# Optimization experiments

Measured on AMD Instinct MI355X. Metric: run time of the kernel, lower is better.

The kernel has to match this reference:

```python
import jax, jax.numpy as jnp
import numpy as np
from jax.scipy.special import logsumexp

B, M, N = 512, 256, 256
ITERS = 20


def setup_inputs() -> dict:
    key = jax.random.key(0)
    k1, = jax.random.split(key, 1)
    scores = jax.random.normal(k1, (B, M, N), dtype=jnp.float32)
    alpha = jnp.ones((1,), dtype=jnp.float32)  # dustbin_weights parameter
    return {"scores": scores, "alpha": alpha, "iters": ITERS}


def reference(scores, alpha, iters):
    b, m, n = scores.shape
    a = alpha.reshape(())
    # Augment with dustbin row/column -> couplings [b, m+1, n+1]
    bins0 = jnp.broadcast_to(a, (b, m, 1))
    bins1 = jnp.broadcast_to(a, (b, 1, n))
    corner = jnp.broadcast_to(a, (b, 1, 1))
    couplings = jnp.concatenate(
        [jnp.concatenate([scores, bins0], axis=2),
         jnp.concatenate([bins1, corner], axis=2)], axis=1)

    ms = jnp.asarray(m, scores.dtype)
    ns = jnp.asarray(n, scores.dtype)
    norm = -jnp.log(ms + ns)  # scalar
    log_mu = jnp.concatenate([jnp.full((m,), norm, scores.dtype),
                              (jnp.log(ns) + norm)[None]])  # [m+1]
    log_nu = jnp.concatenate([jnp.full((n,), norm, scores.dtype),
                              (jnp.log(ms) + norm)[None]])  # [n+1]
    log_mu = jnp.broadcast_to(log_mu[None], (b, m + 1))
    log_nu = jnp.broadcast_to(log_nu[None], (b, n + 1))

    u0 = jnp.zeros_like(log_mu)
    v0 = jnp.zeros_like(log_nu)

    def body(carry, _):
        u, v = carry
        u = log_mu - logsumexp(couplings + v[:, None, :], axis=2)
        v = log_nu - logsumexp(couplings + u[:, :, None], axis=1)
        return (u, v), None

    (u, v), _ = jax.lax.scan(body, (u0, v0), None, length=iters)
    Z = couplings + u[:, :, None] + v[:, None, :]
    return Z - norm
```

## Files before the change

kernel.cpp:

```cpp
#include <hip/hip_runtime.h>


typedef _Float16 half8 __attribute__((ext_vector_type(8)));
typedef float floatx4 __attribute__((ext_vector_type(4)));

constexpr float L2E = 1.4426950408889634f;
constexpr float LN2 = 0.6931471805599453f;

__device__ __forceinline__ float flog2(float x) { return __builtin_amdgcn_logf(x); }
__device__ __forceinline__ float fexp2(float x) { return __builtin_amdgcn_exp2f(x); }

__device__ __forceinline__ float rcp_nr(float d) {
    float r = __builtin_amdgcn_rcpf(d);
    return r * fmaf(-d, r, 2.0f);
}

template <int CTRL>
__device__ __forceinline__ float dpp_add(float x) {
    int y = __builtin_amdgcn_update_dpp(0, __builtin_bit_cast(int, x), CTRL, 0xF, 0xF, true);
    return x + __builtin_bit_cast(float, y);
}
__device__ __forceinline__ float reduce16(float x) {
    x = dpp_add<0xB1>(x);
    x = dpp_add<0x4E>(x);
    x = dpp_add<0x124>(x);
    x = dpp_add<0x128>(x);
    return x;
}
__device__ __forceinline__ float xor16_add(float x) {
    int y = __builtin_amdgcn_ds_swizzle(__builtin_bit_cast(int, x), 0x401F);
    return x + __builtin_bit_cast(float, y);
}

__global__ __launch_bounds__(1024)
__attribute__((amdgpu_waves_per_eu(4, 4)))
void sinkhorn_kernel(const float* __restrict__ scores,
                     const float* __restrict__ alpha_p,
                     const int* __restrict__ iters_p,
                     float* __restrict__ out)
{
    const int bat = blockIdx.x;
    const int t   = threadIdx.x;
    const int a   = t >> 5;
    const int bb  = t & 31;
    const int w   = t >> 6;
    const int l   = t & 63;
    const int g   = (t >> 4) & 3;
    const int l15 = t & 15;

    const float alpha2 = alpha_p[0] * L2E;
    const float A  = fexp2(alpha2);
    const float Cs = fexp2(8.0f - alpha2);
    const int iters = iters_p[0];

    __shared__ __align__(16) unsigned short esT[65536];
    __shared__ __align__(16) unsigned short EUa[272];
    __shared__ __align__(16) unsigned short EVa[272];
    __shared__ __align__(16) float wsU[16];
    __shared__ __align__(16) float wsV[16];

    {
        const float* sp = scores + ((size_t)bat << 16) + ((size_t)a << 11) + (bb << 2);
        half8 cp[8];
        #pragma unroll
        for (int r = 0; r < 8; ++r) {
            const float4 x0 = *reinterpret_cast<const float4*>(sp + (r << 8));
            const float4 x1 = *reinterpret_cast<const float4*>(sp + (r << 8) + 128);
            cp[0][r] = (_Float16)fexp2(x0.x * L2E);
            cp[1][r] = (_Float16)fexp2(x0.y * L2E);
            cp[2][r] = (_Float16)fexp2(x0.z * L2E);
            cp[3][r] = (_Float16)fexp2(x0.w * L2E);
            cp[4][r] = (_Float16)fexp2(x1.x * L2E);
            cp[5][r] = (_Float16)fexp2(x1.y * L2E);
            cp[6][r] = (_Float16)fexp2(x1.z * L2E);
            cp[7][r] = (_Float16)fexp2(x1.w * L2E);
        }
        #pragma unroll
        for (int ci = 0; ci < 8; ++ci) {
            const int col = (ci < 4) ? ((bb << 2) + ci) : (128 + (bb << 2) + ci - 4);
            const int idx = (col << 8) + (((a << 3)) ^ ((col & 7) << 3));
            *reinterpret_cast<half8*>(&esT[idx]) = cp[ci];
        }
    }
    if (t < 256) EVa[t] = 0x3C00;
    if (t < 16)  wsV[t] = 16.0f;
    __syncthreads();

    half8 esA[8];
    {
        const int m16 = (w << 4) + l15;
        #pragma unroll
        for (int s = 0; s < 8; ++s) {
            #pragma unroll
            for (int j = 0; j < 8; ++j) {
                const int col = (s << 5) + (g << 3) + j;
                const unsigned short v =
                    esT[(col << 8) + (m16 ^ ((col & 7) << 3))];
                esA[s][j] = __builtin_bit_cast(_Float16, v);
            }
            asm volatile("" : "+v"(esA[s]));
        }
    }
    half8 esB[8];
    {
        const int cbase = ((w << 4) + l15) << 8;
        const int swq = (l15 & 7) << 3;
        #pragma unroll
        for (int s = 0; s < 8; ++s) {
            esB[s] = *reinterpret_cast<const half8*>(
                &esT[cbase + (((s << 5) + (g << 3)) ^ swq)]);
            asm volatile("" : "+v"(esB[s]));
        }
    }

    float evd = 1.0f, eud_s = 1.0f;

    const half8* evp = reinterpret_cast<const half8*>(EVa) + g;
    const half8* eup = reinterpret_cast<const half8*>(EUa) + g;

    for (int it = 0; it < iters; ++it) {
        float sv = evd;
        {
            const floatx4* wv = reinterpret_cast<const floatx4*>(wsV);
            floatx4 s0 = wv[0], s1 = wv[1], s2 = wv[2], s3 = wv[3];
            floatx4 ss = (s0 + s1) + (s2 + s3);
            sv += (ss[0] + ss[1]) + (ss[2] + ss[3]);
        }
        eud_s = Cs * rcp_nr(sv);
        const float tdu = A * eud_s;
        const float tdv = A * evd;

        floatx4 acc0 = {0.f, 0.f, 0.f, 0.f}, acc1 = {0.f, 0.f, 0.f, 0.f};
        #pragma unroll
        for (int s = 0; s < 4; ++s) {
            acc0 = __builtin_amdgcn_mfma_f32_16x16x32_f16(esA[2*s],   evp[(2*s) << 2],   acc0, 0, 0, 0);
            acc1 = __builtin_amdgcn_mfma_f32_16x16x32_f16(esA[2*s+1], evp[(2*s+1) << 2], acc1, 0, 0, 0);
        }
        floatx4 acc = acc0 + acc1;

        const float E0 = rcp_nr(acc[0] + tdv);
        const float E1 = rcp_nr(acc[1] + tdv);
        const float E2 = rcp_nr(acc[2] + tdv);
        const float E3 = rcp_nr(acc[3] + tdv);
        if (l15 < 4) {
            const float lo  = (l15 & 1) ? E1 : E0;
            const float hi  = (l15 & 1) ? E3 : E2;
            const float val = (l15 & 2) ? hi : lo;
            EUa[(w << 4) + (g << 2) + l15] =
                __builtin_bit_cast(unsigned short, (_Float16)val);
        }
        float sU = (E0 + E1) + (E2 + E3);
        sU = xor16_add(sU);
        sU += __shfl_xor(sU, 32, 64);
        if (l == 0) wsU[w] = sU;
        __syncthreads();

        float su = eud_s;
        {
            const floatx4* wu = reinterpret_cast<const floatx4*>(wsU);
            floatx4 s0 = wu[0], s1 = wu[1], s2 = wu[2], s3 = wu[3];
            floatx4 ss = (s0 + s1) + (s2 + s3);
            su += (ss[0] + ss[1]) + (ss[2] + ss[3]);
        }
        evd = Cs * rcp_nr(su);

        floatx4 q0 = {0.f, 0.f, 0.f, 0.f}, q1 = {0.f, 0.f, 0.f, 0.f};
        #pragma unroll
        for (int s = 0; s < 4; ++s) {
            q0 = __builtin_amdgcn_mfma_f32_16x16x32_f16(eup[(2*s) << 2],   esB[2*s],   q0, 0, 0, 0);
            q1 = __builtin_amdgcn_mfma_f32_16x16x32_f16(eup[(2*s+1) << 2], esB[2*s+1], q1, 0, 0, 0);
        }
        floatx4 acc2 = q0 + q1;

        const float EVv = rcp_nr(acc2[0] + tdu);
        if (l < 16) EVa[(w << 4) + l] =
            __builtin_bit_cast(unsigned short, (_Float16)EVv);
        float sV = reduce16(EVv);
        if (l == 0) wsV[w] = sV;
        __syncthreads();
    }

    half8 evf[8];
    #pragma unroll
    for (int s = 0; s < 8; ++s) evf[s] = evp[s << 2];

    const float Ud = flog2(eud_s);
    const float Vd = flog2(evd);
    const float Up_l = flog2((float)__builtin_bit_cast(_Float16, EUa[(w << 4) + l15]));
    const int row = (w << 4) + l15;
    const size_t ob = (size_t)bat * 66049;
    float* rp = out + ob + (size_t)row * 257;

    #pragma unroll
    for (int s = 0; s < 8; ++s) {
        const int c0 = (s << 5) + (g << 3);
        #pragma unroll
        for (int j = 0; j < 8; ++j) {
            rp[c0 + j] = (flog2((float)esA[s][j]) + Up_l + flog2((float)evf[s][j])) * LN2;
        }
    }
    if (l < 16) rp[256] = (alpha2 + Up_l + Vd) * LN2;
    if (t < 257) {
        const float vp = (t < 256)
            ? flog2((float)__builtin_bit_cast(_Float16, EVa[t])) : Vd;
        out[ob + 65792 + t] = (alpha2 + Ud + vp) * LN2;
    }
}

extern "C" void kernel_launch(void* const* d_in, const int* in_sizes, int n_in,
                              void* d_out, int out_size, void* d_ws, size_t ws_size,
                              hipStream_t stream)
{
    const float* scores = (const float*)d_in[0];
    const float* alpha  = (const float*)d_in[1];
    const int*   iters  = (const int*)d_in[2];
    float* out = (float*)d_out;
    const int B = in_sizes[0] >> 16;
    hipLaunchKernelGGL(sinkhorn_kernel, dim3(B), dim3(1024), 0, stream,
                       scores, alpha, iters, out);
}
```

Baseline: 109.7 us.

## Process two batches per block, prefetching second batch's scores during first loop

Each workgroup now handles two batch items. While the first batch runs its Sinkhorn iterations, the second batch's scores are streamed into LDS in chunks with async global-to-LDS loads, exponentiated and written into the transposed fp16 tile. The goal is to hide the global load latency behind compute. The cost is halving the grid to 256 blocks on a GPU with many CUs, which may underfill the device, and running the two batches back to back. There are also race concerns, because esT is overwritten while the first batch's epilogue and loop still read from it.

```diff
diff --git a/kernel.cpp b/kernel.cpp
--- a/kernel.cpp
+++ b/kernel.cpp
@@ -37,9 +37,8 @@
 void sinkhorn_kernel(const float* __restrict__ scores,
                      const float* __restrict__ alpha_p,
                      const int* __restrict__ iters_p,
-                     float* __restrict__ out)
+                     float* __restrict__ out, int B)
 {
-    const int bat = blockIdx.x;
     const int t   = threadIdx.x;
     const int a   = t >> 5;
     const int bb  = t & 31;
@@ -48,19 +47,27 @@
     const int g   = (t >> 4) & 3;
     const int l15 = t & 15;
 
+    const int bat0 = blockIdx.x << 1;
+    const int bat1 = bat0 + 1;
+    const bool haveB1 = bat1 < B;
+
     const float alpha2 = alpha_p[0] * L2E;
     const float A  = fexp2(alpha2);
     const float Cs = fexp2(8.0f - alpha2);
     const int iters = iters_p[0];
 
     __shared__ __align__(16) unsigned short esT[65536];
+    __shared__ __align__(16) float rawbuf[4096];
     __shared__ __align__(16) unsigned short EUa[272];
     __shared__ __align__(16) unsigned short EVa[272];
     __shared__ __align__(16) float wsU[16];
     __shared__ __align__(16) float wsV[16];
 
+    float evd, eud_s;
+    half8 esA[8], esB[8];
+
     {
-        const float* sp = scores + ((size_t)bat << 16) + ((size_t)a << 11) + (bb << 2);
+        const float* sp = scores + ((size_t)bat0 << 16) + ((size_t)a << 11) + (bb << 2);
         half8 cp[8];
         #pragma unroll
         for (int r = 0; r < 8; ++r) {
@@ -86,23 +93,18 @@
     if (t < 16)  wsV[t] = 16.0f;
     __syncthreads();
 
-    half8 esA[8];
-    {
+    auto gather = [&]() {
         const int m16 = (w << 4) + l15;
         #pragma unroll
         for (int s = 0; s < 8; ++s) {
             #pragma unroll
             for (int j = 0; j < 8; ++j) {
                 const int col = (s << 5) + (g << 3) + j;
-                const unsigned short v =
-                    esT[(col << 8) + (m16 ^ ((col & 7) << 3))];
-                esA[s][j] = __builtin_bit_cast(_Float16, v);
+                esA[s][j] = __builtin_bit_cast(_Float16,
+                    esT[(col << 8) + (m16 ^ ((col & 7) << 3))]);
             }
             asm volatile("" : "+v"(esA[s]));
         }
-    }
-    half8 esB[8];
-    {
         const int cbase = ((w << 4) + l15) << 8;
         const int swq = (l15 & 7) << 3;
         #pragma unroll
@@ -111,100 +113,152 @@
                 &esT[cbase + (((s << 5) + (g << 3)) ^ swq)]);
             asm volatile("" : "+v"(esB[s]));
         }
-    }
-
-    float evd = 1.0f, eud_s = 1.0f;
+    };
+
+    const float* sB1 = scores + ((size_t)bat1 << 16);
+    auto issue_chunk = [&](int c) {
+        const float* gp = sB1 + (c << 12) + (w << 8) + (l << 2);
+        __builtin_amdgcn_global_load_lds(
+            (const __attribute__((address_space(1))) void*)gp,
+            (__attribute__((address_space(3))) void*)&rawbuf[w << 8],
+            16, 0, 0);
+    };
+    auto consume_chunk = [&](int c) {
+        const float4 v = *reinterpret_cast<const float4*>(&rawbuf[t << 2]);
+        const int row   = (c << 4) + (t >> 6);
+        const int cb    = (t & 63) << 2;
+        const int rslot = row & ~7;
+        const int rin   = row & 7;
+        const float vv[4] = {v.x, v.y, v.z, v.w};
+        #pragma unroll
+        for (int cc = 0; cc < 4; ++cc) {
+            const int col = cb + cc;
+            esT[(col << 8) + ((rslot ^ ((col & 7) << 3)) + rin)] =
+                __builtin_bit_cast(unsigned short, (_Float16)fexp2(vv[cc] * L2E));
+        }
+    };
 
     const half8* evp = reinterpret_cast<const half8*>(EVa) + g;
     const half8* eup = reinterpret_cast<const half8*>(EUa) + g;
 
-    for (int it = 0; it < iters; ++it) {
-        float sv = evd;
-        {
-            const floatx4* wv = reinterpret_cast<const floatx4*>(wsV);
-            floatx4 s0 = wv[0], s1 = wv[1], s2 = wv[2], s3 = wv[3];
-            floatx4 ss = (s0 + s1) + (s2 + s3);
-            sv += (ss[0] + ss[1]) + (ss[2] + ss[3]);
-        }
-        eud_s = Cs * rcp_nr(sv);
-        const float tdu = A * eud_s;
-        const float tdv = A * evd;
-
-        floatx4 acc0 = {0.f, 0.f, 0.f, 0.f}, acc1 = {0.f, 0.f, 0.f, 0.f};
-        #pragma unroll
-        for (int s = 0; s < 4; ++s) {
-            acc0 = __builtin_amdgcn_mfma_f32_16x16x32_f16(esA[2*s],   evp[(2*s) << 2],   acc0, 0, 0, 0);
-            acc1 = __builtin_amdgcn_mfma_f32_16x16x32_f16(esA[2*s+1], evp[(2*s+1) << 2], acc1, 0, 0, 0);
-        }
-        floatx4 acc = acc0 + acc1;
-
-        const float E0 = rcp_nr(acc[0] + tdv);
-        const float E1 = rcp_nr(acc[1] + tdv);
-        const float E2 = rcp_nr(acc[2] + tdv);
-        const float E3 = rcp_nr(acc[3] + tdv);
-        if (l15 < 4) {
-            const float lo  = (l15 & 1) ? E1 : E0;
-            const float hi  = (l15 & 1) ? E3 : E2;
-            const float val = (l15 & 2) ? hi : lo;
-            EUa[(w << 4) + (g << 2) + l15] =
-                __builtin_bit_cast(unsigned short, (_Float16)val);
-        }
-        float sU = (E0 + E1) + (E2 + E3);
-        sU = xor16_add(sU);
-        sU += __shfl_xor(sU, 32, 64);
-        if (l == 0) wsU[w] = sU;
-        __syncthreads();
-
-        float su = eud_s;
-        {
-            const floatx4* wu = reinterpret_cast<const floatx4*>(wsU);
-            floatx4 s0 = wu[0], s1 = wu[1], s2 = wu[2], s3 = wu[3];
-            floatx4 ss = (s0 + s1) + (s2 + s3);
-            su += (ss[0] + ss[1]) + (ss[2] + ss[3]);
-        }
-        evd = Cs * rcp_nr(su);
-
-        floatx4 q0 = {0.f, 0.f, 0.f, 0.f}, q1 = {0.f, 0.f, 0.f, 0.f};
-        #pragma unroll
-        for (int s = 0; s < 4; ++s) {
-            q0 = __builtin_amdgcn_mfma_f32_16x16x32_f16(eup[(2*s) << 2],   esB[2*s],   q0, 0, 0, 0);
-            q1 = __builtin_amdgcn_mfma_f32_16x16x32_f16(eup[(2*s+1) << 2], esB[2*s+1], q1, 0, 0, 0);
-        }
-        floatx4 acc2 = q0 + q1;
-
-        const float EVv = rcp_nr(acc2[0] + tdu);
-        if (l < 16) EVa[(w << 4) + l] =
-            __builtin_bit_cast(unsigned short, (_Float16)EVv);
-        float sV = reduce16(EVv);
-        if (l == 0) wsV[w] = sV;
-        __syncthreads();
+    auto run_loop = [&](bool doStage) {
+        evd = 1.0f; eud_s = 1.0f;
+        for (int it = 0; it < iters; ++it) {
+            if (doStage) {
+                if (it >= 1 && it <= 16) {
+                    asm volatile("s_waitcnt vmcnt(0)" ::: "memory");
+                    consume_chunk(it - 1);
+                }
+                if (it <= 15) issue_chunk(it);
+            }
+
+            float sv = evd;
+            {
+                const floatx4* wv = reinterpret_cast<const floatx4*>(wsV);
+                floatx4 s0 = wv[0], s1 = wv[1], s2 = wv[2], s3 = wv[3];
+                floatx4 ss = (s0 + s1) + (s2 + s3);
+                sv += (ss[0] + ss[1]) + (ss[2] + ss[3]);
+            }
+            eud_s = Cs * rcp_nr(sv);
+            const float tdu = A * eud_s;
+            const float tdv = A * evd;
+
+            floatx4 acc0 = {0.f, 0.f, 0.f, 0.f}, acc1 = {0.f, 0.f, 0.f, 0.f};
+            #pragma unroll
+            for (int s = 0; s < 4; ++s) {
+                acc0 = __builtin_amdgcn_mfma_f32_16x16x32_f16(esA[2*s],   evp[(2*s) << 2],   acc0, 0, 0, 0);
+                acc1 = __builtin_amdgcn_mfma_f32_16x16x32_f16(esA[2*s+1], evp[(2*s+1) << 2], acc1, 0, 0, 0);
+            }
+            floatx4 acc = acc0 + acc1;
+
+            const float E0 = rcp_nr(acc[0] + tdv);
+            const float E1 = rcp_nr(acc[1] + tdv);
+            const float E2 = rcp_nr(acc[2] + tdv);
+            const float E3 = rcp_nr(acc[3] + tdv);
+            if (l15 < 4) {
+                const float lo  = (l15 & 1) ? E1 : E0;
+                const float hi  = (l15 & 1) ? E3 : E2;
+                const float val = (l15 & 2) ? hi : lo;
+                EUa[(w << 4) + (g << 2) + l15] =
+                    __builtin_bit_cast(unsigned short, (_Float16)val);
+            }
+            float sU = (E0 + E1) + (E2 + E3);
+            sU = xor16_add(sU);
+            sU += __shfl_xor(sU, 32, 64);
+            if (l == 0) wsU[w] = sU;
+            __syncthreads();
+
+            float su = eud_s;
+            {
+                const floatx4* wu = reinterpret_cast<const floatx4*>(wsU);
+                floatx4 s0 = wu[0], s1 = wu[1], s2 = wu[2], s3 = wu[3];
+                floatx4 ss = (s0 + s1) + (s2 + s3);
+                su += (ss[0] + ss[1]) + (ss[2] + ss[3]);
+            }
+            evd = Cs * rcp_nr(su);
+
+            floatx4 q0 = {0.f, 0.f, 0.f, 0.f}, q1 = {0.f, 0.f, 0.f, 0.f};
+            #pragma unroll
+            for (int s = 0; s < 4; ++s) {
+                q0 = __builtin_amdgcn_mfma_f32_16x16x32_f16(eup[(2*s) << 2],   esB[2*s],   q0, 0, 0, 0);
+                q1 = __builtin_amdgcn_mfma_f32_16x16x32_f16(eup[(2*s+1) << 2], esB[2*s+1], q1, 0, 0, 0);
+            }
+            floatx4 acc2 = q0 + q1;
+
+            const float EVv = rcp_nr(acc2[0] + tdu);
+            if (l < 16) EVa[(w << 4) + l] =
+                __builtin_bit_cast(unsigned short, (_Float16)EVv);
+            float sV = reduce16(EVv);
+            if (l == 0) wsV[w] = sV;
+            __syncthreads();
+        }
+    };
+
+    auto do_epilogue = [&](int bat) {
+        const float Ud = flog2(eud_s);
+        const float Vd = flog2(evd);
+        const float Up_l = flog2((float)__builtin_bit_cast(_Float16, EUa[(w << 4) + l15]));
+        const int row = (w << 4) + l15;
+        const size_t ob = (size_t)bat * 66049;
+        float* rp = out + ob + (size_t)row * 257;
+        #pragma unroll
+        for (int s = 0; s < 8; ++s) {
+            const half8 ev8 = evp[s << 2];
+            const int c0 = (s << 5) + (g << 3);
+            #pragma unroll
+            for (int j = 0; j < 8; ++j)
+                rp[c0 + j] = (flog2((float)esA[s][j]) + Up_l + flog2((float)ev8[j])) * LN2;
+        }
+        if (l < 16) rp[256] = (alpha2 + Up_l + Vd) * LN2;
+        if (t < 257) {
+            const float vp = (t < 256)
+                ? flog2((float)__builtin_bit_cast(_Float16, EVa[t])) : Vd;
+            out[ob + 65792 + t] = (alpha2 + Ud + vp) * LN2;
+        }
+    };
+
+    gather();
+    run_loop(haveB1);
+    if (haveB1) {
+        const int consumed = (iters >= 1) ? ((iters - 1) < 16 ? (iters - 1) : 16) : 0;
+        const int issuedN  = (iters < 16) ? (iters < 0 ? 0 : iters) : 16;
+        for (int c = consumed; c < 16; ++c) {
+            if (c >= issuedN) issue_chunk(c);
+            asm volatile("s_waitcnt vmcnt(0)" ::: "memory");
+            consume_chunk(c);
+        }
     }
-
-    half8 evf[8];
-    #pragma unroll
-    for (int s = 0; s < 8; ++s) evf[s] = evp[s << 2];
-
-    const float Ud = flog2(eud_s);
-    const float Vd = flog2(evd);
-    const float Up_l = flog2((float)__builtin_bit_cast(_Float16, EUa[(w << 4) + l15]));
-    const int row = (w << 4) + l15;
-    const size_t ob = (size_t)bat * 66049;
-    float* rp = out + ob + (size_t)row * 257;
-
-    #pragma unroll
-    for (int s = 0; s < 8; ++s) {
-        const int c0 = (s << 5) + (g << 3);
-        #pragma unroll
-        for (int j = 0; j < 8; ++j) {
-            rp[c0 + j] = (flog2((float)esA[s][j]) + Up_l + flog2((float)evf[s][j])) * LN2;
-        }
-    }
-    if (l < 16) rp[256] = (alpha2 + Up_l + Vd) * LN2;
-    if (t < 257) {
-        const float vp = (t < 256)
-            ? flog2((float)__builtin_bit_cast(_Float16, EVa[t])) : Vd;
-        out[ob + 65792 + t] = (alpha2 + Ud + vp) * LN2;
-    }
+    do_epilogue(bat0);
+
+    if (!haveB1) return;
+
+    __syncthreads();
+    if (t < 256) EVa[t] = 0x3C00;
+    if (t < 16)  wsV[t] = 16.0f;
+    gather();
+    __syncthreads();
+    run_loop(false);
+    do_epilogue(bat1);
 }
 
 extern "C" void kernel_launch(void* const* d_in, const int* in_sizes, int n_in,
@@ -216,6 +270,6 @@
     const int*   iters  = (const int*)d_in[2];
     float* out = (float*)d_out;
     const int B = in_sizes[0] >> 16;
-    hipLaunchKernelGGL(sinkhorn_kernel, dim3(B), dim3(1024), 0, stream,
-                       scores, alpha, iters, out);
-}
+    hipLaunchKernelGGL(sinkhorn_kernel, dim3((B + 1) >> 1), dim3(1024), 0, stream,
+                       scores, alpha, iters, out, B);
+}
```

New measurement: 135.9 us. 23.9% more time.

## Switch Sinkhorn matvecs to FP8 MFMA and drop the LDS transpose staging

Applied to the files above, without the earlier changes.

Stores exp(scores) as e4m3 FP8 in registers and runs both Sinkhorn matrix-vector products with fp8 MFMA, using a x16 scaling factor to keep the values in range. The 128KB LDS transpose buffer is removed: the row-major and transposed operands are each loaded directly from global memory. This lowers LDS use and lets waves_per_eu rise to 8. The final output re-reads the raw scores instead of taking the log of the quantized exponentials. FP8 quantization of the couplings and of the u/v vectors adds substantial numerical error and may break tolerance. The strided global loads for the transposed operand are uncoalesced.

```diff
diff --git a/kernel.cpp b/kernel.cpp
--- a/kernel.cpp
+++ b/kernel.cpp
@@ -1,8 +1,9 @@
 #include <hip/hip_runtime.h>
 
 
-typedef _Float16 half8 __attribute__((ext_vector_type(8)));
 typedef float floatx4 __attribute__((ext_vector_type(4)));
+typedef unsigned int uint2v __attribute__((ext_vector_type(2)));
+typedef _Float16 half8v __attribute__((ext_vector_type(8)));
 
 constexpr float L2E = 1.4426950408889634f;
 constexpr float LN2 = 0.6931471805599453f;
@@ -32,8 +33,33 @@
     return x + __builtin_bit_cast(float, y);
 }
 
+__device__ __forceinline__ unsigned f32_to_e4m3(float x) {
+    if (!(x > 0.0f)) return 0u;
+    if (x < 0.015625f) {
+        int mi = (int)fmaf(x, 512.0f, 0.5f);
+        return (unsigned)mi;
+    }
+    unsigned u = __builtin_bit_cast(unsigned, x);
+    unsigned r = u + 0x80000u;
+    int e2 = (int)((r >> 23) & 255u) - 127;
+    if (e2 > 8) return 0x7Eu;
+    unsigned b = (unsigned)(((e2 + 7) << 3) | ((r >> 20) & 7u));
+    if (b >= 0x7Fu) b = 0x7Eu;
+    return b;
+}
+
+__device__ __forceinline__ long pack8_e4m3(const float* v) {
+    unsigned lo = 0, hi = 0;
+    #pragma unroll
+    for (int j = 0; j < 4; ++j) lo |= f32_to_e4m3(v[j]) << (8 * j);
+    #pragma unroll
+    for (int j = 0; j < 4; ++j) hi |= f32_to_e4m3(v[j + 4]) << (8 * j);
+    uint2v p; p.x = lo; p.y = hi;
+    return __builtin_bit_cast(long, p);
+}
+
 __global__ __launch_bounds__(1024)
-__attribute__((amdgpu_waves_per_eu(4, 4)))
+__attribute__((amdgpu_waves_per_eu(8, 8)))
 void sinkhorn_kernel(const float* __restrict__ scores,
                      const float* __restrict__ alpha_p,
                      const int* __restrict__ iters_p,
@@ -41,8 +67,6 @@
 {
     const int bat = blockIdx.x;
     const int t   = threadIdx.x;
-    const int a   = t >> 5;
-    const int bb  = t & 31;
     const int w   = t >> 6;
     const int l   = t & 63;
     const int g   = (t >> 4) & 3;
@@ -53,70 +77,47 @@
     const float Cs = fexp2(8.0f - alpha2);
     const int iters = iters_p[0];
 
-    __shared__ __align__(16) unsigned short esT[65536];
-    __shared__ __align__(16) unsigned short EUa[272];
-    __shared__ __align__(16) unsigned short EVa[272];
+    __shared__ __align__(16) unsigned char EV8a[288];
+    __shared__ __align__(16) unsigned char EU8a[288];
+    __shared__ __align__(16) unsigned short EUa[288];
+    __shared__ __align__(16) unsigned short EVa[288];
     __shared__ __align__(16) float wsU[16];
     __shared__ __align__(16) float wsV[16];
 
+    const float* S = scores + ((size_t)bat << 16);
+    const int row = (w << 4) + l15;
+
+    long esA[8], esB[8];
     {
-        const float* sp = scores + ((size_t)bat << 16) + ((size_t)a << 11) + (bb << 2);
-        half8 cp[8];
-        #pragma unroll
-        for (int r = 0; r < 8; ++r) {
-            const float4 x0 = *reinterpret_cast<const float4*>(sp + (r << 8));
-            const float4 x1 = *reinterpret_cast<const float4*>(sp + (r << 8) + 128);
-            cp[0][r] = (_Float16)fexp2(x0.x * L2E);
-            cp[1][r] = (_Float16)fexp2(x0.y * L2E);
-            cp[2][r] = (_Float16)fexp2(x0.z * L2E);
-            cp[3][r] = (_Float16)fexp2(x0.w * L2E);
-            cp[4][r] = (_Float16)fexp2(x1.x * L2E);
-            cp[5][r] = (_Float16)fexp2(x1.y * L2E);
-            cp[6][r] = (_Float16)fexp2(x1.z * L2E);
-            cp[7][r] = (_Float16)fexp2(x1.w * L2E);
-        }
-        #pragma unroll
-        for (int ci = 0; ci < 8; ++ci) {
-            const int col = (ci < 4) ? ((bb << 2) + ci) : (128 + (bb << 2) + ci - 4);
-            const int idx = (col << 8) + (((a << 3)) ^ ((col & 7) << 3));
-            *reinterpret_cast<half8*>(&esT[idx]) = cp[ci];
-        }
-    }
+        const float* rowp = S + (row << 8) + (g << 3);
+        #pragma unroll
+        for (int s = 0; s < 8; ++s) {
+            const float4 x0 = *reinterpret_cast<const float4*>(rowp + (s << 5));
+            const float4 x1 = *reinterpret_cast<const float4*>(rowp + (s << 5) + 4);
+            float v[8] = {fexp2(x0.x * L2E), fexp2(x0.y * L2E),
+                          fexp2(x0.z * L2E), fexp2(x0.w * L2E),
+                          fexp2(x1.x * L2E), fexp2(x1.y * L2E),
+                          fexp2(x1.z * L2E), fexp2(x1.w * L2E)};
+            esA[s] = pack8_e4m3(v);
+            asm volatile("" : "+v"(esA[s]));
+        }
+        #pragma unroll
+        for (int s = 0; s < 8; ++s) {
+            const float* cp = S + (((s << 5) + (g << 3)) << 8) + row;
+            float v[8];
+            #pragma unroll
+            for (int j = 0; j < 8; ++j) v[j] = fexp2(cp[j << 8] * L2E);
+            esB[s] = pack8_e4m3(v);
+            asm volatile("" : "+v"(esB[s]));
+        }
+    }
+
+    if (t < 64)  reinterpret_cast<unsigned*>(EV8a)[t] = 0x58585858u;
     if (t < 256) EVa[t] = 0x3C00;
     if (t < 16)  wsV[t] = 16.0f;
     __syncthreads();
 
-    half8 esA[8];
-    {
-        const int m16 = (w << 4) + l15;
-        #pragma unroll
-        for (int s = 0; s < 8; ++s) {
-            #pragma unroll
-            for (int j = 0; j < 8; ++j) {
-                const int col = (s << 5) + (g << 3) + j;
-                const unsigned short v =
-                    esT[(col << 8) + (m16 ^ ((col & 7) << 3))];
-                esA[s][j] = __builtin_bit_cast(_Float16, v);
-            }
-            asm volatile("" : "+v"(esA[s]));
-        }
-    }
-    half8 esB[8];
-    {
-        const int cbase = ((w << 4) + l15) << 8;
-        const int swq = (l15 & 7) << 3;
-        #pragma unroll
-        for (int s = 0; s < 8; ++s) {
-            esB[s] = *reinterpret_cast<const half8*>(
-                &esT[cbase + (((s << 5) + (g << 3)) ^ swq)]);
-            asm volatile("" : "+v"(esB[s]));
-        }
-    }
-
     float evd = 1.0f, eud_s = 1.0f;
-
-    const half8* evp = reinterpret_cast<const half8*>(EVa) + g;
-    const half8* eup = reinterpret_cast<const half8*>(EUa) + g;
 
     for (int it = 0; it < iters; ++it) {
         float sv = evd;
@@ -127,27 +128,30 @@
             sv += (ss[0] + ss[1]) + (ss[2] + ss[3]);
         }
         eud_s = Cs * rcp_nr(sv);
-        const float tdu = A * eud_s;
-        const float tdv = A * evd;
+        const float tdu16 = 16.0f * A * eud_s;
+        const float tdv16 = 16.0f * A * evd;
 
         floatx4 acc0 = {0.f, 0.f, 0.f, 0.f}, acc1 = {0.f, 0.f, 0.f, 0.f};
         #pragma unroll
         for (int s = 0; s < 4; ++s) {
-            acc0 = __builtin_amdgcn_mfma_f32_16x16x32_f16(esA[2*s],   evp[(2*s) << 2],   acc0, 0, 0, 0);
-            acc1 = __builtin_amdgcn_mfma_f32_16x16x32_f16(esA[2*s+1], evp[(2*s+1) << 2], acc1, 0, 0, 0);
-        }
-        floatx4 acc = acc0 + acc1;
-
-        const float E0 = rcp_nr(acc[0] + tdv);
-        const float E1 = rcp_nr(acc[1] + tdv);
-        const float E2 = rcp_nr(acc[2] + tdv);
-        const float E3 = rcp_nr(acc[3] + tdv);
+            const long b0 = *reinterpret_cast<const long*>(&EV8a[((2*s) << 5) + (g << 3)]);
+            const long b1 = *reinterpret_cast<const long*>(&EV8a[((2*s+1) << 5) + (g << 3)]);
+            acc0 = __builtin_amdgcn_mfma_f32_16x16x32_fp8_fp8(esA[2*s],   b0, acc0, 0, 0, 0);
+            acc1 = __builtin_amdgcn_mfma_f32_16x16x32_fp8_fp8(esA[2*s+1], b1, acc1, 0, 0, 0);
+        }
+        const floatx4 acc = acc0 + acc1;
+
+        const float E0 = 16.0f * rcp_nr(acc[0] + tdv16);
+        const float E1 = 16.0f * rcp_nr(acc[1] + tdv16);
+        const float E2 = 16.0f * rcp_nr(acc[2] + tdv16);
+        const float E3 = 16.0f * rcp_nr(acc[3] + tdv16);
         if (l15 < 4) {
             const float lo  = (l15 & 1) ? E1 : E0;
             const float hi  = (l15 & 1) ? E3 : E2;
             const float val = (l15 & 2) ? hi : lo;
-            EUa[(w << 4) + (g << 2) + l15] =
-                __builtin_bit_cast(unsigned short, (_Float16)val);
+            const int idx = (w << 4) + (g << 2) + l15;
+            EUa[idx]  = __builtin_bit_cast(unsigned short, (_Float16)val);
+            EU8a[idx] = (unsigned char)f32_to_e4m3(val * 16.0f);
         }
         float sU = (E0 + E1) + (E2 + E3);
         sU = xor16_add(sU);
@@ -167,37 +171,40 @@
         floatx4 q0 = {0.f, 0.f, 0.f, 0.f}, q1 = {0.f, 0.f, 0.f, 0.f};
         #pragma unroll
         for (int s = 0; s < 4; ++s) {
-            q0 = __builtin_amdgcn_mfma_f32_16x16x32_f16(eup[(2*s) << 2],   esB[2*s],   q0, 0, 0, 0);
-            q1 = __builtin_amdgcn_mfma_f32_16x16x32_f16(eup[(2*s+1) << 2], esB[2*s+1], q1, 0, 0, 0);
-        }
-        floatx4 acc2 = q0 + q1;
-
-        const float EVv = rcp_nr(acc2[0] + tdu);
-        if (l < 16) EVa[(w << 4) + l] =
-            __builtin_bit_cast(unsigned short, (_Float16)EVv);
+            const long a0 = *reinterpret_cast<const long*>(&EU8a[((2*s) << 5) + (g << 3)]);
+            const long a1 = *reinterpret_cast<const long*>(&EU8a[((2*s+1) << 5) + (g << 3)]);
+            q0 = __builtin_amdgcn_mfma_f32_16x16x32_fp8_fp8(a0, esB[2*s],   q0, 0, 0, 0);
+            q1 = __builtin_amdgcn_mfma_f32_16x16x32_fp8_fp8(a1, esB[2*s+1], q1, 0, 0, 0);
+        }
+        const floatx4 acc2 = q0 + q1;
+
+        const float EVv = 16.0f * rcp_nr(acc2[0] + tdu16);
+        if (l < 16) {
+            EVa[(w << 4) + l]  = __builtin_bit_cast(unsigned short, (_Float16)EVv);
+            EV8a[(w << 4) + l] = (unsigned char)f32_to_e4m3(EVv * 16.0f);
+        }
         float sV = reduce16(EVv);
         if (l == 0) wsV[w] = sV;
         __syncthreads();
     }
 
-    half8 evf[8];
-    #pragma unroll
-    for (int s = 0; s < 8; ++s) evf[s] = evp[s << 2];
-
     const float Ud = flog2(eud_s);
     const float Vd = flog2(evd);
     const float Up_l = flog2((float)__builtin_bit_cast(_Float16, EUa[(w << 4) + l15]));
-    const int row = (w << 4) + l15;
     const size_t ob = (size_t)bat * 66049;
     float* rp = out + ob + (size_t)row * 257;
+    const float* rowp = S + (row << 8) + (g << 3);
 
     #pragma unroll
     for (int s = 0; s < 8; ++s) {
+        const float4 x0 = *reinterpret_cast<const float4*>(rowp + (s << 5));
+        const float4 x1 = *reinterpret_cast<const float4*>(rowp + (s << 5) + 4);
+        const half8v vh = *reinterpret_cast<const half8v*>(&EVa[(s << 5) + (g << 3)]);
         const int c0 = (s << 5) + (g << 3);
-        #pragma unroll
-        for (int j = 0; j < 8; ++j) {
-            rp[c0 + j] = (flog2((float)esA[s][j]) + Up_l + flog2((float)evf[s][j])) * LN2;
-        }
+        const float xs[8] = {x0.x, x0.y, x0.z, x0.w, x1.x, x1.y, x1.z, x1.w};
+        #pragma unroll
+        for (int j = 0; j < 8; ++j)
+            rp[c0 + j] = (xs[j] * L2E + Up_l + flog2((float)vh[j])) * LN2;
     }
     if (l < 16) rp[256] = (alpha2 + Up_l + Vd) * LN2;
     if (t < 257) {
```

Measured after the change: 185.2 us. 1.69x slower.

## Use FP8 MFMA for Sinkhorn matvecs and process two batches per block

Applied to the files above, without the earlier changes.

Converts the exp-score matrices held in registers from fp16 to fp8 e4m3 and switches the iteration matvecs to fp8 MFMA, keeping fp16 copies of the scaling vectors for the epilogue. Each block now handles two batch items interleaved in the iteration loop, halving the grid and sharing each barrier between two independent problems. The goal is to cut barrier and latency overhead per batch and halve register footprint per matrix. In exchange, precision drops sharply: the output log-couplings are decoded from fp8 scores, which risks tolerance failures.

```diff
diff --git a/kernel.cpp b/kernel.cpp
--- a/kernel.cpp
+++ b/kernel.cpp
@@ -3,6 +3,7 @@
 
 typedef _Float16 half8 __attribute__((ext_vector_type(8)));
 typedef float floatx4 __attribute__((ext_vector_type(4)));
+typedef unsigned int uint2v __attribute__((ext_vector_type(2)));
 
 constexpr float L2E = 1.4426950408889634f;
 constexpr float LN2 = 0.6931471805599453f;
@@ -21,15 +22,59 @@
     return x + __builtin_bit_cast(float, y);
 }
 __device__ __forceinline__ float reduce16(float x) {
-    x = dpp_add<0xB1>(x);
-    x = dpp_add<0x4E>(x);
-    x = dpp_add<0x124>(x);
-    x = dpp_add<0x128>(x);
+    x = dpp_add<0xB1>(x); x = dpp_add<0x4E>(x);
+    x = dpp_add<0x124>(x); x = dpp_add<0x128>(x);
     return x;
 }
 __device__ __forceinline__ float xor16_add(float x) {
     int y = __builtin_amdgcn_ds_swizzle(__builtin_bit_cast(int, x), 0x401F);
     return x + __builtin_bit_cast(float, y);
+}
+
+__device__ __forceinline__ unsigned f32_to_e4m3(float x) {
+    if (!(x > 0.0f)) return 0u;
+    if (x < 0.015625f) return (unsigned)(int)fmaf(x, 512.0f, 0.5f);
+    unsigned u = __builtin_bit_cast(unsigned, x);
+    unsigned r = u + 0x80000u;
+    int e2 = (int)((r >> 23) & 255u) - 127;
+    if (e2 > 8) return 0x7Eu;
+    unsigned b = (unsigned)(((e2 + 7) << 3) | ((r >> 20) & 7u));
+    if (b >= 0x7Fu) b = 0x7Eu;
+    return b;
+}
+__device__ __forceinline__ float dec_e4m3(unsigned b) {
+    unsigned e = (b >> 3) & 15u, m = b & 7u;
+    if (e == 0) return (float)m * 0.001953125f;
+    return __builtin_bit_cast(float, ((e + 120u) << 23) | (m << 20));
+}
+
+__device__ __forceinline__ long h8_to_fp8(half8 h) {
+    unsigned lo, hi;
+#if __has_builtin(__builtin_amdgcn_cvt_pk_fp8_f32)
+    lo = (unsigned)__builtin_amdgcn_cvt_pk_fp8_f32((float)h[0], (float)h[1], 0, false);
+    lo = (unsigned)__builtin_amdgcn_cvt_pk_fp8_f32((float)h[2], (float)h[3], (int)lo, true);
+    hi = (unsigned)__builtin_amdgcn_cvt_pk_fp8_f32((float)h[4], (float)h[5], 0, false);
+    hi = (unsigned)__builtin_amdgcn_cvt_pk_fp8_f32((float)h[6], (float)h[7], (int)hi, true);
+#else
+    lo = 0; hi = 0;
+    #pragma unroll
+    for (int j = 0; j < 4; ++j) lo |= f32_to_e4m3((float)h[j]) << (j << 3);
+    #pragma unroll
+    for (int j = 0; j < 4; ++j) hi |= f32_to_e4m3((float)h[j + 4]) << (j << 3);
+#endif
+    uint2v p; p.x = lo; p.y = hi;
+    return __builtin_bit_cast(long, p);
+}
+__device__ __forceinline__ unsigned f32_to_fp8b(float x) {
+#if __has_builtin(__builtin_amdgcn_cvt_pk_fp8_f32)
+    return (unsigned)__builtin_amdgcn_cvt_pk_fp8_f32(x, 0.0f, 0, false) & 255u;
+#else
+    return f32_to_e4m3(x);
+#endif
+}
+
+__device__ __forceinline__ int eidx(int col, int r) {
+    return col * 264 + ((r ^ ((col & 7) << 3)) + (((col >> 3) & 1) << 3));
 }
 
 __global__ __launch_bounds__(1024)
@@ -37,9 +82,8 @@
 void sinkhorn_kernel(const float* __restrict__ scores,
                      const float* __restrict__ alpha_p,
                      const int* __restrict__ iters_p,
-                     float* __restrict__ out)
+                     float* __restrict__ out, int B)
 {
-    const int bat = blockIdx.x;
     const int t   = threadIdx.x;
     const int a   = t >> 5;
     const int bb  = t & 31;
@@ -48,18 +92,23 @@
     const int g   = (t >> 4) & 3;
     const int l15 = t & 15;
 
+    const int bat0 = blockIdx.x << 1;
+    const bool haveB1 = (bat0 + 1) < B;
+    const int bat1 = haveB1 ? (bat0 + 1) : bat0;
+
     const float alpha2 = alpha_p[0] * L2E;
     const float A  = fexp2(alpha2);
     const float Cs = fexp2(8.0f - alpha2);
     const int iters = iters_p[0];
 
-    __shared__ __align__(16) unsigned short esT[65536];
-    __shared__ __align__(16) unsigned short EUa[272];
-    __shared__ __align__(16) unsigned short EVa[272];
-    __shared__ __align__(16) float wsU[16];
-    __shared__ __align__(16) float wsV[16];
-
-    {
+    __shared__ __align__(16) unsigned short esT[256 * 264];
+    __shared__ __align__(16) unsigned char  EV80[288], EV81[288];
+    __shared__ __align__(16) unsigned char  EU80[288], EU81[288];
+    __shared__ __align__(16) unsigned short EVh0[288], EVh1[288];
+    __shared__ __align__(16) unsigned short EUh0[288], EUh1[288];
+    __shared__ __align__(16) float wsU0[16], wsU1[16], wsV0[16], wsV1[16];
+
+    auto stage = [&](int bat) {
         const float* sp = scores + ((size_t)bat << 16) + ((size_t)a << 11) + (bb << 2);
         half8 cp[8];
         #pragma unroll
@@ -78,133 +127,173 @@
         #pragma unroll
         for (int ci = 0; ci < 8; ++ci) {
             const int col = (ci < 4) ? ((bb << 2) + ci) : (128 + (bb << 2) + ci - 4);
-            const int idx = (col << 8) + (((a << 3)) ^ ((col & 7) << 3));
-            *reinterpret_cast<half8*>(&esT[idx]) = cp[ci];
-        }
-    }
-    if (t < 256) EVa[t] = 0x3C00;
-    if (t < 16)  wsV[t] = 16.0f;
-    __syncthreads();
-
-    half8 esA[8];
-    {
+            *reinterpret_cast<half8*>(&esT[eidx(col, a << 3)]) = cp[ci];
+        }
+    };
+
+    long esA0[8], esB0[8], esA1[8], esB1[8];
+    auto gather = [&](long* eA, long* eB) {
         const int m16 = (w << 4) + l15;
         #pragma unroll
         for (int s = 0; s < 8; ++s) {
+            half8 cp;
             #pragma unroll
             for (int j = 0; j < 8; ++j) {
                 const int col = (s << 5) + (g << 3) + j;
-                const unsigned short v =
-                    esT[(col << 8) + (m16 ^ ((col & 7) << 3))];
-                esA[s][j] = __builtin_bit_cast(_Float16, v);
+                cp[j] = __builtin_bit_cast(_Float16, esT[eidx(col, m16)]);
             }
-            asm volatile("" : "+v"(esA[s]));
-        }
+            eA[s] = h8_to_fp8(cp);
+            asm volatile("" : "+v"(eA[s]));
+        }
+        #pragma unroll
+        for (int s = 0; s < 8; ++s) {
+            const half8 hb = *reinterpret_cast<const half8*>(
+                &esT[eidx(m16, (s << 5) + (g << 3))]);
+            eB[s] = h8_to_fp8(hb);
+            asm volatile("" : "+v"(eB[s]));
+        }
+    };
+
+    stage(bat0);
+    __syncthreads();
+    gather(esA0, esB0);
+    __syncthreads();
+    stage(bat1);
+    if (t < 64) {
+        reinterpret_cast<unsigned*>(EV80)[t] = 0x58585858u;
+        reinterpret_cast<unsigned*>(EV81)[t] = 0x58585858u;
     }
-    half8 esB[8];
-    {
-        const int cbase = ((w << 4) + l15) << 8;
-        const int swq = (l15 & 7) << 3;
-        #pragma unroll
-        for (int s = 0; s < 8; ++s) {
-            esB[s] = *reinterpret_cast<const half8*>(
-                &esT[cbase + (((s << 5) + (g << 3)) ^ swq)]);
-            asm volatile("" : "+v"(esB[s]));
-        }
-    }
-
-    float evd = 1.0f, eud_s = 1.0f;
-
-    const half8* evp = reinterpret_cast<const half8*>(EVa) + g;
-    const half8* eup = reinterpret_cast<const half8*>(EUa) + g;
+    if (t < 256) { EVh0[t] = 0x3C00; EVh1[t] = 0x3C00; }
+    if (t < 16)  { wsV0[t] = 16.0f; wsV1[t] = 16.0f; }
+    __syncthreads();
+    gather(esA1, esB1);
+
+    float evd0 = 1.0f, eud0 = 1.0f, evd1 = 1.0f, eud1 = 1.0f;
 
     for (int it = 0; it < iters; ++it) {
-        float sv = evd;
+        float sv0 = evd0, sv1 = evd1;
         {
-            const floatx4* wv = reinterpret_cast<const floatx4*>(wsV);
-            floatx4 s0 = wv[0], s1 = wv[1], s2 = wv[2], s3 = wv[3];
-            floatx4 ss = (s0 + s1) + (s2 + s3);
-            sv += (ss[0] + ss[1]) + (ss[2] + ss[3]);
-        }
-        eud_s = Cs * rcp_nr(sv);
-        const float tdu = A * eud_s;
-        const float tdv = A * evd;
-
-        floatx4 acc0 = {0.f, 0.f, 0.f, 0.f}, acc1 = {0.f, 0.f, 0.f, 0.f};
+            const floatx4* p0 = reinterpret_cast<const floatx4*>(wsV0);
+            const floatx4* p1 = reinterpret_cast<const floatx4*>(wsV1);
+            floatx4 s0 = (p0[0] + p0[1]) + (p0[2] + p0[3]);
+            floatx4 s1 = (p1[0] + p1[1]) + (p1[2] + p1[3]);
+            sv0 += (s0[0] + s0[1]) + (s0[2] + s0[3]);
+            sv1 += (s1[0] + s1[1]) + (s1[2] + s1[3]);
+        }
+        eud0 = Cs * rcp_nr(sv0);
+        eud1 = Cs * rcp_nr(sv1);
+        const float tdu0 = 16.0f * A * eud0, tdv0 = 16.0f * A * evd0;
+        const float tdu1 = 16.0f * A * eud1, tdv1 = 16.0f * A * evd1;
+
+        floatx4 c00 = {0,0,0,0}, c01 = {0,0,0,0}, c10 = {0,0,0,0}, c11 = {0,0,0,0};
         #pragma unroll
         for (int s = 0; s < 4; ++s) {
-            acc0 = __builtin_amdgcn_mfma_f32_16x16x32_f16(esA[2*s],   evp[(2*s) << 2],   acc0, 0, 0, 0);
-            acc1 = __builtin_amdgcn_mfma_f32_16x16x32_f16(esA[2*s+1], evp[(2*s+1) << 2], acc1, 0, 0, 0);
-        }
-        floatx4 acc = acc0 + acc1;
-
-        const float E0 = rcp_nr(acc[0] + tdv);
-        const float E1 = rcp_nr(acc[1] + tdv);
-        const float E2 = rcp_nr(acc[2] + tdv);
-        const float E3 = rcp_nr(acc[3] + tdv);
+            const long b00 = *reinterpret_cast<const long*>(&EV80[((2*s) << 5) + (g << 3)]);
+            const long b01 = *reinterpret_cast<const long*>(&EV80[((2*s+1) << 5) + (g << 3)]);
+            const long b10 = *reinterpret_cast<const long*>(&EV81[((2*s) << 5) + (g << 3)]);
+            const long b11 = *reinterpret_cast<const long*>(&EV81[((2*s+1) << 5) + (g << 3)]);
+            c00 = __builtin_amdgcn_mfma_f32_16x16x32_fp8_fp8(esA0[2*s],   b00, c00, 0, 0, 0);
+            c01 = __builtin_amdgcn_mfma_f32_16x16x32_fp8_fp8(esA0[2*s+1], b01, c01, 0, 0, 0);
+            c10 = __builtin_amdgcn_mfma_f32_16x16x32_fp8_fp8(esA1[2*s],   b10, c10, 0, 0, 0);
+            c11 = __builtin_amdgcn_mfma_f32_16x16x32_fp8_fp8(esA1[2*s+1], b11, c11, 0, 0, 0);
+        }
+        const floatx4 ap0 = c00 + c01;
+        const floatx4 ap1 = c10 + c11;
+
+        float E0[4], E1[4];
+        #pragma unroll
+        for (int i = 0; i < 4; ++i) {
+            E0[i] = 16.0f * rcp_nr(ap0[i] + tdv0);
+            E1[i] = 16.0f * rcp_nr(ap1[i] + tdv1);
+        }
         if (l15 < 4) {
-            const float lo  = (l15 & 1) ? E1 : E0;
-            const float hi  = (l15 & 1) ? E3 : E2;
-            const float val = (l15 & 2) ? hi : lo;
-            EUa[(w << 4) + (g << 2) + l15] =
-                __builtin_bit_cast(unsigned short, (_Float16)val);
-        }
-        float sU = (E0 + E1) + (E2 + E3);
-        sU = xor16_add(sU);
-        sU += __shfl_xor(sU, 32, 64);
-        if (l == 0) wsU[w] = sU;
+            const float v0 = (l15 & 2) ? ((l15 & 1) ? E0[3] : E0[2])
+                                       : ((l15 & 1) ? E0[1] : E0[0]);
+            const float v1 = (l15 & 2) ? ((l15 & 1) ? E1[3] : E1[2])
+                                       : ((l15 & 1) ? E1[1] : E1[0]);
+            const int i0 = (w << 4) + (g << 2) + l15;
+            EUh0[i0] = __builtin_bit_cast(unsigned short, (_Float16)v0);
+            EU80[i0] = (unsigned char)f32_to_fp8b(v0 * 16.0f);
+            EUh1[i0] = __builtin_bit_cast(unsigned short, (_Float16)v1);
+            EU81[i0] = (unsigned char)f32_to_fp8b(v1 * 16.0f);
+        }
+        float sU0 = (E0[0] + E0[1]) + (E0[2] + E0[3]);
+        float sU1 = (E1[0] + E1[1]) + (E1[2] + E1[3]);
+        sU0 = xor16_add(sU0); sU0 += __shfl_xor(sU0, 32, 64);
+        sU1 = xor16_add(sU1); sU1 += __shfl_xor(sU1, 32, 64);
+        if (l == 0) { wsU0[w] = sU0; wsU1[w] = sU1; }
         __syncthreads();
 
-        float su = eud_s;
+        float su0 = eud0, su1 = eud1;
         {
-            const floatx4* wu = reinterpret_cast<const floatx4*>(wsU);
-            floatx4 s0 = wu[0], s1 = wu[1], s2 = wu[2], s3 = wu[3];
-            floatx4 ss = (s0 + s1) + (s2 + s3);
-            su += (ss[0] + ss[1]) + (ss[2] + ss[3]);
-        }
-        evd = Cs * rcp_nr(su);
-
-        floatx4 q0 = {0.f, 0.f, 0.f, 0.f}, q1 = {0.f, 0.f, 0.f, 0.f};
+            const floatx4* p0 = reinterpret_cast<const floatx4*>(wsU0);
+            const floatx4* p1 = reinterpret_cast<const floatx4*>(wsU1);
+            floatx4 s0 = (p0[0] + p0[1]) + (p0[2] + p0[3]);
+            floatx4 s1 = (p1[0] + p1[1]) + (p1[2] + p1[3]);
+            su0 += (s0[0] + s0[1]) + (s0[2] + s0[3]);
+            su1 += (s1[0] + s1[1]) + (s1[2] + s1[3]);
+        }
+        evd0 = Cs * rcp_nr(su0);
+        evd1 = Cs * rcp_nr(su1);
+
+        floatx4 q00 = {0,0,0,0}, q01 = {0,0,0,0}, q10 = {0,0,0,0}, q11 = {0,0,0,0};
         #pragma unroll
         for (int s = 0; s < 4; ++s) {
-            q0 = __builtin_amdgcn_mfma_f32_16x16x32_f16(eup[(2*s) << 2],   esB[2*s],   q0, 0, 0, 0);
-            q1 = __builtin_amdgcn_mfma_f32_16x16x32_f16(eup[(2*s+1) << 2], esB[2*s+1], q1, 0, 0, 0);
-        }
-        floatx4 acc2 = q0 + q1;
-
-        const float EVv = rcp_nr(acc2[0] + tdu);
-        if (l < 16) EVa[(w << 4) + l] =
-            __builtin_bit_cast(unsigned short, (_Float16)EVv);
-        float sV = reduce16(EVv);
-        if (l == 0) wsV[w] = sV;
+            const long a00 = *reinterpret_cast<const long*>(&EU80[((2*s) << 5) + (g << 3)]);
+            const long a01 = *reinterpret_cast<const long*>(&EU80[((2*s+1) << 5) + (g << 3)]);
+            const long a10 = *reinterpret_cast<const long*>(&EU81[((2*s) << 5) + (g << 3)]);
+            const long a11 = *reinterpret_cast<const long*>(&EU81[((2*s+1) << 5) + (g << 3)]);
+            q00 = __builtin_amdgcn_mfma_f32_16x16x32_fp8_fp8(a00, esB0[2*s],   q00, 0, 0, 0);
+            q01 = __builtin_amdgcn_mfma_f32_16x16x32_fp8_fp8(a01, esB0[2*s+1], q01, 0, 0, 0);
+            q10 = __builtin_amdgcn_mfma_f32_16x16x32_fp8_fp8(a10, esB1[2*s],   q10, 0, 0, 0);
+            q11 = __builtin_amdgcn_mfma_f32_16x16x32_fp8_fp8(a11, esB1[2*s+1], q11, 0, 0, 0);
+        }
+        const floatx4 aq0 = q00 + q01;
+        const floatx4 aq1 = q10 + q11;
+
+        const float EVv0 = 16.0f * rcp_nr(aq0[0] + tdu0);
+        const float EVv1 = 16.0f * rcp_nr(aq1[0] + tdu1);
+        if (l < 16) {
+            EVh0[(w << 4) + l] = __builtin_bit_cast(unsigned short, (_Float16)EVv0);
+            EV80[(w << 4) + l] = (unsigned char)f32_to_fp8b(EVv0 * 16.0f);
+            EVh1[(w << 4) + l] = __builtin_bit_cast(unsigned short, (_Float16)EVv1);
+            EV81[(w << 4) + l] = (unsigned char)f32_to_fp8b(EVv1 * 16.0f);
+        }
+        const float sV0 = reduce16(EVv0);
+        const float sV1 = reduce16(EVv1);
+        if (l == 0) { wsV0[w] = sV0; wsV1[w] = sV1; }
         __syncthreads();
     }
 
-    half8 evf[8];
-    #pragma unroll
-    for (int s = 0; s < 8; ++s) evf[s] = evp[s << 2];
-
-    const float Ud = flog2(eud_s);
-    const float Vd = flog2(evd);
-    const float Up_l = flog2((float)__builtin_bit_cast(_Float16, EUa[(w << 4) + l15]));
-    const int row = (w << 4) + l15;
-    const size_t ob = (size_t)bat * 66049;
-    float* rp = out + ob + (size_t)row * 257;
-
-    #pragma unroll
-    for (int s = 0; s < 8; ++s) {
-        const int c0 = (s << 5) + (g << 3);
-        #pragma unroll
-        for (int j = 0; j < 8; ++j) {
-            rp[c0 + j] = (flog2((float)esA[s][j]) + Up_l + flog2((float)evf[s][j])) * LN2;
-        }
-    }
-    if (l < 16) rp[256] = (alpha2 + Up_l + Vd) * LN2;
-    if (t < 257) {
-        const float vp = (t < 256)
-            ? flog2((float)__builtin_bit_cast(_Float16, EVa[t])) : Vd;
-        out[ob + 65792 + t] = (alpha2 + Ud + vp) * LN2;
-    }
+    auto epi = [&](int bat, const long* eA, const unsigned short* EUh,
+                   const unsigned short* EVh, float eud_, float evd_) {
+        const int row = (w << 4) + l15;
+        const float Ud = flog2(eud_);
+        const float Vd = flog2(evd_);
+        const float Up = flog2((float)__builtin_bit_cast(_Float16, EUh[row]));
+        const size_t ob = (size_t)bat * 66049;
+        float* rp = out + ob + (size_t)row * 257;
+        #pragma unroll
+        for (int s = 0; s < 8; ++s) {
+            const uint2v pa = __builtin_bit_cast(uint2v, eA[s]);
+            const half8 vh = *reinterpret_cast<const half8*>(&EVh[(s << 5) + (g << 3)]);
+            const int c0 = (s << 5) + (g << 3);
+            #pragma unroll
+            for (int j = 0; j < 8; ++j) {
+                const unsigned b = (pa[j >> 2] >> ((j & 3) * 8)) & 255u;
+                rp[c0 + j] = (flog2(dec_e4m3(b)) + Up + flog2((float)vh[j])) * LN2;
+            }
+        }
+        if (l < 16) rp[256] = (alpha2 + Up + Vd) * LN2;
+        if (t < 257) {
+            const float vp = (t < 256)
+                ? flog2((float)__builtin_bit_cast(_Float16, EVh[t])) : Vd;
+            out[ob + 65792 + t] = (alpha2 + Ud + vp) * LN2;
+        }
+    };
+
+    epi(bat0, esA0, EUh0, EVh0, eud0, evd0);
+    if (haveB1) epi(bat1, esA1, EUh1, EVh1, eud1, evd1);
 }
 
 extern "C" void kernel_launch(void* const* d_in, const int* in_sizes, int n_in,
@@ -216,6 +305,6 @@
     const int*   iters  = (const int*)d_in[2];
     float* out = (float*)d_out;
     const int B = in_sizes[0] >> 16;
-    hipLaunchKernelGGL(sinkhorn_kernel, dim3(B), dim3(1024), 0, stream,
-                       scores, alpha, iters, out);
-}
+    hipLaunchKernelGGL(sinkhorn_kernel, dim3((B + 1) >> 1), dim3(1024), 0, stream,
+                       scores, alpha, iters, out, B);
+}
```

New measurement: 182.6 us. 66.5% more time.
